# Kernel tuning notes

Hardware: AMD Instinct MI355X
Metric: run time of the kernel (lower is better)

The kernel has to match this reference:

```python
import jax, jax.numpy as jnp
import numpy as np

N = 50000
NEG_SLOPE = 0.2  # PyG GATConv default negative_slope


def _gat_layer(x, src, dst, edge_attr, W, We, a_src, a_dst, a_edge, bias):
    """Single-head PyG GATConv (heads=1, concat=True, add_self_loops=True,
    fill_value='mean' for self-loop edge_attr, dropout inactive / eval mode)."""
    n = x.shape[0]
    # add self loops; self-loop edge_attr = per-feature mean of edge_attr
    loop = jnp.arange(n)
    src2 = jnp.concatenate([src, loop])
    dst2 = jnp.concatenate([dst, loop])
    ea_loop = jnp.broadcast_to(edge_attr.mean(axis=0, keepdims=True), (n, edge_attr.shape[1]))
    ea = jnp.concatenate([edge_attr, ea_loop], axis=0)          # [E', edge_dim]

    h = x @ W                                                    # [N, C_out]
    a_s = h @ a_src                                              # [N]
    a_d = h @ a_dst                                              # [N]
    a_e = (ea @ We) @ a_edge                                     # [E']

    alpha = jax.nn.leaky_relu(a_s[src2] + a_d[dst2] + a_e, NEG_SLOPE)  # [E']
    # segment softmax over incoming edges of each dst node
    amax = jax.ops.segment_max(alpha, dst2, num_segments=n)     # [N]
    ex = jnp.exp(alpha - amax[dst2])                             # [E']
    denom = jax.ops.segment_sum(ex, dst2, num_segments=n)       # [N]
    w = ex / denom[dst2]                                         # [E']

    msg = h[src2] * w[:, None]                                   # [E', C_out]
    out = jax.ops.segment_sum(msg, dst2, num_segments=n) + bias  # [N, C_out]
    return out


def setup_inputs() -> dict:
    key = jax.random.key(0)
    ks = jax.random.split(key, 16)
    E, C_in, C_h, C_out, Ed = 800000, 128, 256, 128, 8
    s = 0.05
    inp = {
        "x": jax.random.normal(ks[0], (N, C_in), dtype=jnp.float32),
        "edge_index": jax.random.randint(ks[1], (2, E), 0, N, dtype=jnp.int32),
        "edge_attr": jax.random.normal(ks[2], (E, Ed), dtype=jnp.float32),
        # layer 1 params
        "W1": jax.random.normal(ks[3], (C_in, C_h), dtype=jnp.float32) * s,
        "We1": jax.random.normal(ks[4], (Ed, C_h), dtype=jnp.float32) * s,
        "as1": jax.random.normal(ks[5], (C_h,), dtype=jnp.float32) * s,
        "ad1": jax.random.normal(ks[6], (C_h,), dtype=jnp.float32) * s,
        "ae1": jax.random.normal(ks[7], (C_h,), dtype=jnp.float32) * s,
        "b1": jnp.zeros((C_h,), dtype=jnp.float32),
        # layer 2 params
        "W2": jax.random.normal(ks[8], (C_h, C_out), dtype=jnp.float32) * s,
        "We2": jax.random.normal(ks[9], (Ed, C_out), dtype=jnp.float32) * s,
        "as2": jax.random.normal(ks[10], (C_out,), dtype=jnp.float32) * s,
        "ad2": jax.random.normal(ks[11], (C_out,), dtype=jnp.float32) * s,
        "ae2": jax.random.normal(ks[12], (C_out,), dtype=jnp.float32) * s,
        "b2": jnp.zeros((C_out,), dtype=jnp.float32),
    }
    return inp


def reference(x, edge_index, edge_attr, W1, We1, as1, ad1, ae1, b1,
              W2, We2, as2, ad2, ae2, b2):
    src, dst = edge_index[0], edge_index[1]
    h = _gat_layer(x, src, dst, edge_attr, W1, We1, as1, ad1, ae1, b1)
    h = jax.nn.relu(h)  # relu between layers, not after last
    out = _gat_layer(h, src, dst, edge_attr, W2, We2, as2, ad2, ae2, b2)
    return out
```

## Files before the change

### kernel.cpp

```cpp
#include <hip/hip_runtime.h>
#include <hip/hip_bf16.h>


#define NEG_SLOPE 0.2f

typedef unsigned short u16;
typedef short short8 __attribute__((ext_vector_type(8)));
typedef float v4f __attribute__((ext_vector_type(4)));
typedef u16 u16x4 __attribute__((ext_vector_type(4)));
typedef u16 u16x8 __attribute__((ext_vector_type(8)));

__device__ __forceinline__ u16 f2bf(float f) {
    unsigned u = __float_as_uint(f);
    return (u16)((u + 0x7fffu + ((u >> 16) & 1u)) >> 16);
}
__device__ __forceinline__ float bf2f(u16 h) {
    return __uint_as_float(((unsigned)h) << 16);
}
__device__ __forceinline__ float bf_lo(int v) { return __uint_as_float(((unsigned)v) << 16); }
__device__ __forceinline__ float bf_hi(int v) { return __uint_as_float(((unsigned)v) & 0xffff0000u); }
__device__ __forceinline__ float lrelu(float x) {
    return x >= 0.f ? x : NEG_SLOPE * x;
}
__device__ __forceinline__ int ld_acq(int* p) {
    return __hip_atomic_load(p, __ATOMIC_ACQUIRE, __HIP_MEMORY_SCOPE_AGENT);
}
__device__ __forceinline__ void st_rel(int* p, int v) {
    __hip_atomic_store(p, v, __ATOMIC_RELEASE, __HIP_MEMORY_SCOPE_AGENT);
}

__global__ __launch_bounds__(256) void prep_kernel(
        const float* __restrict__ W1, u16* __restrict__ w1thi, u16* __restrict__ w1tlo,
        const float* __restrict__ W2, u16* __restrict__ w2thi, u16* __restrict__ w2tlo,
        const float* __restrict__ We1, const float* __restrict__ ae1v,
        const float* __restrict__ We2, const float* __restrict__ ae2v,
        float* __restrict__ we_vec1g, float* __restrict__ we_vec2g) {
    int tid = threadIdx.x;
    if (blockIdx.x < 256) {
        int t = blockIdx.x * 256 + tid;
        if (t < 128 * 256) {
            int k = t >> 8, m = t & 255;
            float v = W1[t];
            u16 h = f2bf(v);
            w1thi[(size_t)m * 128 + k] = h;
            w1tlo[(size_t)m * 128 + k] = f2bf(v - bf2f(h));
        } else {
            t -= 128 * 256;
            int k = t >> 7, m = t & 127;
            float v = W2[t];
            u16 h = f2bf(v);
            w2thi[(size_t)m * 256 + k] = h;
            w2tlo[(size_t)m * 256 + k] = f2bf(v - bf2f(h));
        }
        return;
    }
    __shared__ float wv[16];
    if (tid < 16) wv[tid] = 0.f;
    __syncthreads();
    {
        float a1 = ae1v[tid];
        int lane = tid & 63;
#pragma unroll
        for (int j = 0; j < 8; ++j) {
            float v = We1[j * 256 + tid] * a1;
#pragma unroll
            for (int o = 32; o; o >>= 1) v += __shfl_down(v, o);
            if (lane == 0) atomicAdd(&wv[j], v);
        }
        if (tid < 128) {
            float a2 = ae2v[tid];
#pragma unroll
            for (int j = 0; j < 8; ++j) {
                float v = We2[j * 128 + tid] * a2;
#pragma unroll
                for (int o = 32; o; o >>= 1) v += __shfl_down(v, o);
                if (lane == 0) atomicAdd(&wv[8 + j], v);
            }
        }
    }
    __syncthreads();
    if (tid < 8)  we_vec1g[tid] = wv[tid];
    else if (tid < 16) we_vec2g[tid - 8] = wv[tid];
}

#define BK 32
#define LDA 40
__global__ __launch_bounds__(256) void fat1_kernel(
        const float* __restrict__ ea, const int* __restrict__ dst,
        float* __restrict__ mean_acc, int* __restrict__ deg,
        int* __restrict__ rank, float2* __restrict__ aEe, int E,
        const float* __restrict__ we_vec1g, const float* __restrict__ we_vec2g,
        int Fb, int Gg,
        const float* __restrict__ A32,
        const u16* __restrict__ Bh_g, const u16* __restrict__ Bl_g,
        u16* __restrict__ Cb, int Nrows, int K, int M,
        const float* __restrict__ av, const float* __restrict__ bv,
        float* __restrict__ as_out, float* __restrict__ ad_out, int gx) {
    __shared__ u16 Ah[64 * LDA];
    __shared__ u16 Bh[128 * LDA];
    __shared__ u16 Bl[128 * LDA];
    __shared__ float red[8];
    int tid = threadIdx.x;
    int bid = (int)blockIdx.x;
    int mn = Fb < Gg ? Fb : Gg;
    int hid = -1, gid = -1;
    if (bid < 2 * mn) {
        if ((bid & 1) == 0) hid = bid >> 1; else gid = bid >> 1;
    } else {
        int rem = bid - 2 * mn;
        if (Fb > Gg) hid = mn + rem; else gid = mn + rem;
    }
    if (hid >= 0) {
        float wv[16];
#pragma unroll
        for (int j = 0; j < 8; ++j) { wv[j] = we_vec1g[j]; wv[8 + j] = we_vec2g[j]; }
        if (tid < 8) red[tid] = 0.f;
        __syncthreads();
        float s[8] = {0.f};
        int stride = Fb * 256;
        for (int e = hid * 256 + tid; e < E; e += stride) {
            int d = dst[e];
            const float4 v0 = *(const float4*)&ea[(size_t)e * 8];
            const float4 v1 = *(const float4*)&ea[(size_t)e * 8 + 4];
            s[0] += v0.x; s[1] += v0.y; s[2] += v0.z; s[3] += v0.w;
            s[4] += v1.x; s[5] += v1.y; s[6] += v1.z; s[7] += v1.w;
            float s1 = v0.x * wv[0] + v0.y * wv[1] + v0.z * wv[2] + v0.w * wv[3]
                     + v1.x * wv[4] + v1.y * wv[5] + v1.z * wv[6] + v1.w * wv[7];
            float s2 = v0.x * wv[8] + v0.y * wv[9] + v0.z * wv[10] + v0.w * wv[11]
                     + v1.x * wv[12] + v1.y * wv[13] + v1.z * wv[14] + v1.w * wv[15];
            aEe[e] = make_float2(s1, s2);
            rank[e] = atomicAdd(&deg[d], 1);
        }
        int lane = tid & 63;
#pragma unroll
        for (int j = 0; j < 8; ++j) {
#pragma unroll
            for (int o = 32; o; o >>= 1) s[j] += __shfl_down(s[j], o);
            if (lane == 0) atomicAdd(&red[j], s[j]);
        }
        __syncthreads();
        if (tid < 8) atomicAdd(&mean_acc[tid], red[tid]);
        return;
    }
    int lane = tid & 63;
    int wvx = tid >> 6;
    int l15 = lane & 15, quad = lane >> 4;
    int rb = (gid / gx) * 64;
    int cb = (gid % gx) * 128;

    v4f acc[8];
#pragma unroll
    for (int ni = 0; ni < 8; ++ni) acc[ni] = (v4f){0.f, 0.f, 0.f, 0.f};

    int sr  = tid >> 2;
    int sc  = (tid & 3) * 8;
    int sr2 = tid >> 1;
    int sc2 = (tid & 1) * 16;

    for (int kc = 0; kc < K; kc += BK) {
        int gr = rb + sr;
        u16x8 a0 = {0,0,0,0,0,0,0,0};
        if (gr < Nrows) {
            const float* pa = A32 + (size_t)gr * K + kc + sc;
            float4 f0 = *(const float4*)pa;
            float4 f1 = *(const float4*)(pa + 4);
            a0 = (u16x8){f2bf(f0.x), f2bf(f0.y), f2bf(f0.z), f2bf(f0.w),
                         f2bf(f1.x), f2bf(f1.y), f2bf(f1.z), f2bf(f1.w)};
        }
        size_t bb = (size_t)(cb + sr2) * K + kc + sc2;
        u16x8 b0 = *(const u16x8*)(Bh_g + bb);
        u16x8 b1 = *(const u16x8*)(Bh_g + bb + 8);
        u16x8 b2 = *(const u16x8*)(Bl_g + bb);
        u16x8 b3 = *(const u16x8*)(Bl_g + bb + 8);
        *(u16x8*)&Ah[sr * LDA + sc] = a0;
        *(u16x8*)&Bh[sr2 * LDA + sc2] = b0;
        *(u16x8*)&Bh[sr2 * LDA + sc2 + 8] = b1;
        *(u16x8*)&Bl[sr2 * LDA + sc2] = b2;
        *(u16x8*)&Bl[sr2 * LDA + sc2 + 8] = b3;
        __syncthreads();
        short8 ah = *(const short8*)&Ah[(wvx * 16 + l15) * LDA + quad * 8];
#pragma unroll
        for (int ni = 0; ni < 8; ++ni) {
            int r = (ni * 16 + l15) * LDA + quad * 8;
            short8 bhf = *(const short8*)&Bh[r];
            short8 blf = *(const short8*)&Bl[r];
            acc[ni] = __builtin_amdgcn_mfma_f32_16x16x32_bf16(ah, bhf, acc[ni], 0, 0, 0);
            acc[ni] = __builtin_amdgcn_mfma_f32_16x16x32_bf16(ah, blf, acc[ni], 0, 0, 0);
        }
        __syncthreads();
    }
#pragma unroll
    for (int ni = 0; ni < 8; ++ni)
#pragma unroll
        for (int reg = 0; reg < 4; ++reg) {
            int row = rb + wvx * 16 + quad * 4 + reg;
            if (row < Nrows)
                Cb[(size_t)row * M + cb + ni * 16 + l15] = f2bf(acc[ni][reg]);
        }
    float sd[4] = {}, dd[4] = {};
#pragma unroll
    for (int ni = 0; ni < 8; ++ni) {
        int col = cb + ni * 16 + l15;
        float a = av[col], b = bv[col];
#pragma unroll
        for (int reg = 0; reg < 4; ++reg) {
            sd[reg] += acc[ni][reg] * a;
            dd[reg] += acc[ni][reg] * b;
        }
    }
#pragma unroll
    for (int off = 1; off < 16; off <<= 1)
#pragma unroll
        for (int reg = 0; reg < 4; ++reg) {
            sd[reg] += __shfl_xor(sd[reg], off);
            dd[reg] += __shfl_xor(dd[reg], off);
        }
    if (l15 == 0) {
        int row0 = rb + wvx * 16 + quad * 4;
#pragma unroll
        for (int reg = 0; reg < 4; ++reg)
            if (row0 + reg < Nrows) {
                atomicAdd(as_out + row0 + reg, sd[reg]);
                atomicAdd(ad_out + row0 + reg, dd[reg]);
            }
    }
}

__global__ __launch_bounds__(256) void scan_fused_kernel(
        const int* __restrict__ deg, int* __restrict__ row_start,
        int* __restrict__ partials, int* __restrict__ pprefix,
        int* __restrict__ gcount, int* __restrict__ gflag, int N, int n,
        const float* __restrict__ mean_acc, float Einv,
        const float* __restrict__ we_vec1, const float* __restrict__ we_vec2,
        float* __restrict__ ae_loop) {
    __shared__ int s[256];
    __shared__ int amLast, bprefix;
    int t = threadIdx.x, bid = blockIdx.x;
    int i = bid * 256 + t;
    int v = (i < N) ? deg[i] : 0;
    s[t] = v; __syncthreads();
    for (int off = 1; off < 256; off <<= 1) {
        int u = (t >= off) ? s[t - off] : 0;
        __syncthreads();
        s[t] += u;
        __syncthreads();
    }
    int incl = s[t];
    int total = s[255];
    if (t == 0) {
        partials[bid] = total;
        __threadfence();
        int c = __hip_atomic_fetch_add(gcount, 1, __ATOMIC_ACQ_REL, __HIP_MEMORY_SCOPE_AGENT);
        amLast = (c == (int)gridDim.x - 1);
    }
    __syncthreads();
    if (amLast) {
        int G = gridDim.x;
        int pv = (t < G) ? ld_acq(&partials[t]) : 0;
        __syncthreads();
        s[t] = pv; __syncthreads();
        for (int off = 1; off < 256; off <<= 1) {
            int u = (t >= off) ? s[t - off] : 0;
            __syncthreads();
            s[t] += u;
            __syncthreads();
        }
        if (t < G) pprefix[t] = s[t] - pv;
        if (t == 0) {
            float s1 = 0.f, s2 = 0.f;
#pragma unroll
            for (int j = 0; j < 8; ++j) {
                float m = mean_acc[j] * Einv;
                s1 += m * we_vec1[j];
                s2 += m * we_vec2[j];
            }
            ae_loop[0] = s1; ae_loop[1] = s2;
        }
        __threadfence();
        __syncthreads();
        if (t == 0) st_rel(gflag, 1);
    }
    if (t == 0) {
        while (ld_acq(gflag) == 0) __builtin_amdgcn_s_sleep(2);
        bprefix = ld_acq(&pprefix[bid]);
    }
    __syncthreads();
    int ex = bprefix + incl - v;
    if (i < n) row_start[i] = ex;
}

__global__ __launch_bounds__(256) void fill_kernel(
        const int* __restrict__ src, const int* __restrict__ dst,
        const float2* __restrict__ aEe, const int* __restrict__ row_start,
        const int* __restrict__ rank,
        float4* __restrict__ epack, int E) {
    int e = blockIdx.x * 256 + threadIdx.x;
    if (e >= E) return;
    int d = dst[e];
    int idx = row_start[d] + rank[e];
    float2 a = aEe[e];
    epack[idx] = make_float4(__int_as_float(src[e]), a.x, a.y, 0.f);
}

#define LDA2 40
__global__ __launch_bounds__(256) void gemm_mfma_kernel(
        const u16* __restrict__ A_g,
        const u16* __restrict__ Bh_g, const u16* __restrict__ Bl_g,
        u16* __restrict__ Cb, int Nrows, int K, int M,
        const float* __restrict__ av, const float* __restrict__ bv,
        float* __restrict__ as_out, float* __restrict__ ad_out) {
    __shared__ u16 Ah[128 * LDA2], Bh[128 * LDA2], Bl[128 * LDA2];
    int tid = threadIdx.x;
    int lane = tid & 63;
    int wv = tid >> 6;
    int wm = wv >> 1, wn = wv & 1;
    int l15 = lane & 15, quad = lane >> 4;
    int rb = blockIdx.y * 128;
    int cb = blockIdx.x * 128;

    v4f acc[4][4];
#pragma unroll
    for (int mi = 0; mi < 4; ++mi)
#pragma unroll
        for (int ni = 0; ni < 4; ++ni) acc[mi][ni] = (v4f){0.f, 0.f, 0.f, 0.f};

    int sr = tid >> 1;
    int sc = (tid & 1) * 16;

    for (int kc = 0; kc < K; kc += BK) {
        int gr = rb + sr;
        u16x8 a0 = {0,0,0,0,0,0,0,0}, a1 = {0,0,0,0,0,0,0,0};
        if (gr < Nrows) {
            size_t ba = (size_t)gr * K + kc + sc;
            a0 = *(const u16x8*)(A_g + ba);
            a1 = *(const u16x8*)(A_g + ba + 8);
        }
        size_t bb = (size_t)(cb + sr) * K + kc + sc;
        u16x8 b0 = *(const u16x8*)(Bh_g + bb);
        u16x8 b1 = *(const u16x8*)(Bh_g + bb + 8);
        u16x8 b2 = *(const u16x8*)(Bl_g + bb);
        u16x8 b3 = *(const u16x8*)(Bl_g + bb + 8);
        *(u16x8*)&Ah[sr * LDA2 + sc] = a0;
        *(u16x8*)&Ah[sr * LDA2 + sc + 8] = a1;
        *(u16x8*)&Bh[sr * LDA2 + sc] = b0;
        *(u16x8*)&Bh[sr * LDA2 + sc + 8] = b1;
        *(u16x8*)&Bl[sr * LDA2 + sc] = b2;
        *(u16x8*)&Bl[sr * LDA2 + sc + 8] = b3;
        __syncthreads();
        short8 ah[4], bh[4], bl[4];
#pragma unroll
        for (int mi = 0; mi < 4; ++mi)
            ah[mi] = *(const short8*)&Ah[(wm * 64 + mi * 16 + l15) * LDA2 + quad * 8];
#pragma unroll
        for (int ni = 0; ni < 4; ++ni) {
            int r = (wn * 64 + ni * 16 + l15) * LDA2 + quad * 8;
            bh[ni] = *(const short8*)&Bh[r];
            bl[ni] = *(const short8*)&Bl[r];
        }
#pragma unroll
        for (int mi = 0; mi < 4; ++mi)
#pragma unroll
            for (int ni = 0; ni < 4; ++ni) {
                acc[mi][ni] = __builtin_amdgcn_mfma_f32_16x16x32_bf16(ah[mi], bh[ni], acc[mi][ni], 0, 0, 0);
                acc[mi][ni] = __builtin_amdgcn_mfma_f32_16x16x32_bf16(ah[mi], bl[ni], acc[mi][ni], 0, 0, 0);
            }
        __syncthreads();
    }
#pragma unroll
    for (int mi = 0; mi < 4; ++mi)
#pragma unroll
        for (int ni = 0; ni < 4; ++ni)
#pragma unroll
            for (int reg = 0; reg < 4; ++reg) {
                int row = rb + wm * 64 + mi * 16 + quad * 4 + reg;
                if (row < Nrows)
                    Cb[(size_t)row * M + cb + wn * 64 + ni * 16 + l15] = f2bf(acc[mi][ni][reg]);
            }
    float sd[4][4] = {}, dd[4][4] = {};
#pragma unroll
    for (int ni = 0; ni < 4; ++ni) {
        int col = cb + wn * 64 + ni * 16 + l15;
        float a = av[col], b = bv[col];
#pragma unroll
        for (int mi = 0; mi < 4; ++mi)
#pragma unroll
            for (int reg = 0; reg < 4; ++reg) {
                sd[mi][reg] += acc[mi][ni][reg] * a;
                dd[mi][reg] += acc[mi][ni][reg] * b;
            }
    }
#pragma unroll
    for (int off = 1; off < 16; off <<= 1)
#pragma unroll
        for (int mi = 0; mi < 4; ++mi)
#pragma unroll
            for (int reg = 0; reg < 4; ++reg) {
                sd[mi][reg] += __shfl_xor(sd[mi][reg], off);
                dd[mi][reg] += __shfl_xor(dd[mi][reg], off);
            }
    if (l15 == 0)
#pragma unroll
        for (int mi = 0; mi < 4; ++mi) {
            int row0 = rb + wm * 64 + mi * 16 + quad * 4;
#pragma unroll
            for (int reg = 0; reg < 4; ++reg)
                if (row0 + reg < Nrows) {
                    atomicAdd(as_out + row0 + reg, sd[mi][reg]);
                    atomicAdd(ad_out + row0 + reg, dd[mi][reg]);
                }
        }
}

__global__ __launch_bounds__(256) void agg1_kernel(const int* __restrict__ row_start,
                                                   const float4* __restrict__ epack,
                                                   const float* __restrict__ asv,
                                                   const float* __restrict__ adv,
                                                   const float* __restrict__ ae_loop,
                                                   const u16* __restrict__ Hb,
                                                   u16* __restrict__ ohi,
                                                   const float* __restrict__ bias, int N) {
    __shared__ float2 xch[4][64];
    int lane = threadIdx.x & 63;
    int wvi = threadIdx.x >> 6;
    int node = blockIdx.x * 4 + wvi;
    if (node >= N) return;
    int st = row_start[node], en = row_start[node + 1];
    float ad = adv[node];
    float aloop = lrelu(asv[node] + ad + ae_loop[0]);
    float m = aloop, sum = 1.f;
    float acc0, acc1, acc2, acc3;
    {
        int2 hv = *(const int2*)(Hb + (size_t)node * 256 + lane * 4);
        acc0 = bf_lo(hv.x); acc1 = bf_hi(hv.x);
        acc2 = bf_lo(hv.y); acc3 = bf_hi(hv.y);
    }
    for (int base = st; base < en; base += 64) {
        int i = base + lane;
        float al = -3.0e38f; int sreg = 0;
        if (i < en) {
            float4 ep = epack[i];
            sreg = __float_as_int(ep.x);
            al = lrelu(asv[sreg] + ad + ep.y);
        }
        float cm = al;
#pragma unroll
        for (int o = 1; o < 64; o <<= 1) cm = fmaxf(cm, __shfl_xor(cm, o));
        if (cm > m) {
            float sc = __expf(m - cm);
            acc0 *= sc; acc1 *= sc; acc2 *= sc; acc3 *= sc;
            sum *= sc; m = cm;
        }
        float w = (i < en) ? __expf(al - m) : 0.f;
        float wsum = w;
#pragma unroll
        for (int o = 1; o < 64; o <<= 1) wsum += __shfl_xor(wsum, o);
        sum += wsum;
        xch[wvi][lane] = make_float2(w, __int_as_float(sreg));
        int cnt = min(64, en - base);
        int j = 0;
        for (; j + 8 <= cnt; j += 8) {
            float2 e[8]; int2 h[8];
#pragma unroll
            for (int q = 0; q < 8; ++q) e[q] = xch[wvi][j + q];
#pragma unroll
            for (int q = 0; q < 8; ++q)
                h[q] = *(const int2*)(Hb + (size_t)__float_as_int(e[q].y) * 256 + lane * 4);
#pragma unroll
            for (int q = 0; q < 8; ++q) {
                acc0 += e[q].x * bf_lo(h[q].x); acc1 += e[q].x * bf_hi(h[q].x);
                acc2 += e[q].x * bf_lo(h[q].y); acc3 += e[q].x * bf_hi(h[q].y);
            }
        }
        for (; j + 4 <= cnt; j += 4) {
            float2 e0 = xch[wvi][j], e1 = xch[wvi][j + 1];
            float2 e2 = xch[wvi][j + 2], e3 = xch[wvi][j + 3];
            int2 h0 = *(const int2*)(Hb + (size_t)__float_as_int(e0.y) * 256 + lane * 4);
            int2 h1 = *(const int2*)(Hb + (size_t)__float_as_int(e1.y) * 256 + lane * 4);
            int2 h2 = *(const int2*)(Hb + (size_t)__float_as_int(e2.y) * 256 + lane * 4);
            int2 h3 = *(const int2*)(Hb + (size_t)__float_as_int(e3.y) * 256 + lane * 4);
            acc0 += e0.x * bf_lo(h0.x) + e1.x * bf_lo(h1.x) + e2.x * bf_lo(h2.x) + e3.x * bf_lo(h3.x);
            acc1 += e0.x * bf_hi(h0.x) + e1.x * bf_hi(h1.x) + e2.x * bf_hi(h2.x) + e3.x * bf_hi(h3.x);
            acc2 += e0.x * bf_lo(h0.y) + e1.x * bf_lo(h1.y) + e2.x * bf_lo(h2.y) + e3.x * bf_lo(h3.y);
            acc3 += e0.x * bf_hi(h0.y) + e1.x * bf_hi(h1.y) + e2.x * bf_hi(h2.y) + e3.x * bf_hi(h3.y);
        }
        for (; j < cnt; ++j) {
            float2 e0 = xch[wvi][j];
            int2 h0 = *(const int2*)(Hb + (size_t)__float_as_int(e0.y) * 256 + lane * 4);
            acc0 += e0.x * bf_lo(h0.x); acc1 += e0.x * bf_hi(h0.x);
            acc2 += e0.x * bf_lo(h0.y); acc3 += e0.x * bf_hi(h0.y);
        }
    }
    float inv = 1.f / sum;
    const float4 bvv = *(const float4*)(bias + lane * 4);
    float t0 = acc0 * inv + bvv.x, t1 = acc1 * inv + bvv.y;
    float t2 = acc2 * inv + bvv.z, t3 = acc3 * inv + bvv.w;
    t0 = t0 > 0.f ? t0 : 0.f; t1 = t1 > 0.f ? t1 : 0.f;
    t2 = t2 > 0.f ? t2 : 0.f; t3 = t3 > 0.f ? t3 : 0.f;
    u16x4 h;
    h.x = f2bf(t0); h.y = f2bf(t1); h.z = f2bf(t2); h.w = f2bf(t3);
    *(u16x4*)(ohi + (size_t)node * 256 + lane * 4) = h;
}

__global__ __launch_bounds__(256) void agg2_kernel(const int* __restrict__ row_start,
                                                   const float4* __restrict__ epack,
                                                   const float* __restrict__ asv,
                                                   const float* __restrict__ adv,
                                                   const float* __restrict__ ae_loop,
                                                   const u16* __restrict__ Hb,
                                                   float* __restrict__ out,
                                                   const float* __restrict__ bias, int N) {
    __shared__ float2 xch[4][64];
    int lane = threadIdx.x & 63;
    int wvi = threadIdx.x >> 6;
    int node = blockIdx.x * 4 + wvi;
    if (node >= N) return;
    int st = row_start[node], en = row_start[node + 1];
    float ad = adv[node];
    float aloop = lrelu(asv[node] + ad + ae_loop[1]);
    float m = aloop, sum = 1.f;
    float acc0, acc1;
    {
        int hv = *(const int*)(Hb + (size_t)node * 128 + lane * 2);
        acc0 = bf_lo(hv); acc1 = bf_hi(hv);
    }
    for (int base = st; base < en; base += 64) {
        int i = base + lane;
        float al = -3.0e38f; int sreg = 0;
        if (i < en) {
            float4 ep = epack[i];
            sreg = __float_as_int(ep.x);
            al = lrelu(asv[sreg] + ad + ep.z);
        }
        float cm = al;
#pragma unroll
        for (int o = 1; o < 64; o <<= 1) cm = fmaxf(cm, __shfl_xor(cm, o));
        if (cm > m) {
            float sc = __expf(m - cm);
            acc0 *= sc; acc1 *= sc;
            sum *= sc; m = cm;
        }
        float w = (i < en) ? __expf(al - m) : 0.f;
        float wsum = w;
#pragma unroll
        for (int o = 1; o < 64; o <<= 1) wsum += __shfl_xor(wsum, o);
        sum += wsum;
        xch[wvi][lane] = make_float2(w, __int_as_float(sreg));
        int cnt = min(64, en - base);
        int j = 0;
        for (; j + 8 <= cnt; j += 8) {
            float2 e[8]; int h[8];
#pragma unroll
            for (int q = 0; q < 8; ++q) e[q] = xch[wvi][j + q];
#pragma unroll
            for (int q = 0; q < 8; ++q)
                h[q] = *(const int*)(Hb + (size_t)__float_as_int(e[q].y) * 128 + lane * 2);
#pragma unroll
            for (int q = 0; q < 8; ++q) {
                acc0 += e[q].x * bf_lo(h[q]); acc1 += e[q].x * bf_hi(h[q]);
            }
        }
        for (; j + 4 <= cnt; j += 4) {
            float2 e0 = xch[wvi][j], e1 = xch[wvi][j + 1];
            float2 e2 = xch[wvi][j + 2], e3 = xch[wvi][j + 3];
            int h0 = *(const int*)(Hb + (size_t)__float_as_int(e0.y) * 128 + lane * 2);
            int h1 = *(const int*)(Hb + (size_t)__float_as_int(e1.y) * 128 + lane * 2);
            int h2 = *(const int*)(Hb + (size_t)__float_as_int(e2.y) * 128 + lane * 2);
            int h3 = *(const int*)(Hb + (size_t)__float_as_int(e3.y) * 128 + lane * 2);
            acc0 += e0.x * bf_lo(h0) + e1.x * bf_lo(h1) + e2.x * bf_lo(h2) + e3.x * bf_lo(h3);
            acc1 += e0.x * bf_hi(h0) + e1.x * bf_hi(h1) + e2.x * bf_hi(h2) + e3.x * bf_hi(h3);
        }
        for (; j < cnt; ++j) {
            float2 e0 = xch[wvi][j];
            int h0 = *(const int*)(Hb + (size_t)__float_as_int(e0.y) * 128 + lane * 2);
            acc0 += e0.x * bf_lo(h0); acc1 += e0.x * bf_hi(h0);
        }
    }
    float inv = 1.f / sum;
    size_t o = (size_t)node * 128 + lane * 2;
    out[o]     = acc0 * inv + bias[lane * 2];
    out[o + 1] = acc1 * inv + bias[lane * 2 + 1];
}

extern "C" void kernel_launch(void* const* d_in, const int* in_sizes, int n_in,
                              void* d_out, int out_size, void* d_ws, size_t ws_size,
                              hipStream_t stream) {
    const int Cin = 128, Ch = 256, Co = 128;
    const int N = in_sizes[0] / Cin;
    const int E = in_sizes[1] / 2;

    const float* x   = (const float*)d_in[0];
    const int*   src = (const int*)d_in[1];
    const int*   dst = src + E;
    const float* ea  = (const float*)d_in[2];
    const float* W1  = (const float*)d_in[3];
    const float* We1 = (const float*)d_in[4];
    const float* as1 = (const float*)d_in[5];
    const float* ad1 = (const float*)d_in[6];
    const float* ae1 = (const float*)d_in[7];
    const float* b1  = (const float*)d_in[8];
    const float* W2  = (const float*)d_in[9];
    const float* We2 = (const float*)d_in[10];
    const float* as2 = (const float*)d_in[11];
    const float* ad2 = (const float*)d_in[12];
    const float* ae2 = (const float*)d_in[13];
    const float* b2  = (const float*)d_in[14];
    float* out = (float*)d_out;

    float* ws = (float*)d_ws;
    size_t off = 0;
    u16* h1b = (u16*)(ws + off); off += (size_t)N * Ch / 2;
    u16* g1b = (u16*)(ws + off); off += (size_t)N * Ch / 2;
    float4* epack = (float4*)(ws + off); off += (size_t)E * 4;
    float2* aEe   = (float2*)(ws + off); off += (size_t)E * 2;
    int* rank     = (int*)(ws + off); off += (size_t)E;
    int* row_start = (int*)(ws + off); off += (size_t)N + 1;
    int* partials  = (int*)(ws + off); off += 256;
    int* pprefix   = (int*)(ws + off); off += 256;
    u16* w1thi = (u16*)(ws + off); off += (size_t)Cin * Ch / 2;
    u16* w1tlo = (u16*)(ws + off); off += (size_t)Cin * Ch / 2;
    u16* w2thi = (u16*)(ws + off); off += (size_t)Ch * Co / 2;
    u16* w2tlo = (u16*)(ws + off); off += (size_t)Ch * Co / 2;
    int*   deg  = (int*)(ws + off); off += (size_t)N + 1;
    float* asv1 = ws + off; off += (size_t)N;
    float* adv1 = ws + off; off += (size_t)N;
    float* asv2 = ws + off; off += (size_t)N;
    float* adv2 = ws + off; off += (size_t)N;
    float* misc = ws + off; off += 32;
    float* mean_acc = misc;
    float* we_vec1  = misc + 8;
    float* we_vec2  = misc + 16;
    float* ae_loop  = misc + 24;
    int* gcount = (int*)(ws + off); off += 1;
    int* gflag  = (int*)(ws + off); off += 1;

    const int n1 = N + 1;
    const int nscan = (n1 + 255) / 256;

    hipMemsetAsync(deg, 0, ((size_t)5 * N + 35) * sizeof(float), stream);

    prep_kernel<<<257, 256, 0, stream>>>(
        W1, w1thi, w1tlo, W2, w2thi, w2tlo,
        We1, ae1, We2, ae2, we_vec1, we_vec2);

    {
        int Fb = 1024;
        int gx = Ch / 128;
        int Gg = gx * ((N + 63) / 64);
        fat1_kernel<<<Fb + Gg, 256, 0, stream>>>(
            ea, dst, mean_acc, deg, rank, aEe, E, we_vec1, we_vec2, Fb, Gg,
            x, w1thi, w1tlo, h1b, N, Cin, Ch, as1, ad1, asv1, adv1, gx);
    }

    scan_fused_kernel<<<nscan, 256, 0, stream>>>(
        deg, row_start, partials, pprefix, gcount, gflag, N, n1,
        mean_acc, 1.0f / (float)E, we_vec1, we_vec2, ae_loop);

    fill_kernel<<<(E + 255) / 256, 256, 0, stream>>>(src, dst, aEe, row_start,
                                                     rank, epack, E);

    agg1_kernel<<<(N + 3) / 4, 256, 0, stream>>>(row_start, epack, asv1, adv1, ae_loop,
                                                 h1b, g1b, b1, N);

    u16* h2b = h1b;
    {
        dim3 grid(Co / 128, (N + 127) / 128);
        gemm_mfma_kernel<<<grid, 256, 0, stream>>>(g1b, w2thi, w2tlo, h2b, N, Ch, Co,
                                                   as2, ad2, asv2, adv2);
    }
    agg2_kernel<<<(N + 3) / 4, 256, 0, stream>>>(row_start, epack, asv2, adv2, ae_loop,
                                                 h2b, out, b2, N);
}
```

Measured before the change: 349.8 us.

## Drop online softmax max, precompute layer-1 edge weights in fill, split waves into halves

The running-max online softmax in both aggregation kernels is replaced by a plain exp-sum, which removes the per-chunk max shuffle reduction and the rescaling of accumulators. The layer-1 edge weights exp(lrelu(...)) are now computed once in fill_kernel and stored in epack, so agg1 reads them directly. Each wave is split into two 32-lane halves that gather alternate neighbours with wider vector loads (int4 or int2), and the halves are combined with one cross-half shuffle at the end. Skipping max subtraction risks overflow in exp if attention logits are large, though the small parameter scale probably keeps them bounded.

```diff
diff --git a/kernel.cpp b/kernel.cpp
--- a/kernel.cpp
+++ b/kernel.cpp
@@ -7,7 +7,6 @@
 typedef unsigned short u16;
 typedef short short8 __attribute__((ext_vector_type(8)));
 typedef float v4f __attribute__((ext_vector_type(4)));
-typedef u16 u16x4 __attribute__((ext_vector_type(4)));
 typedef u16 u16x8 __attribute__((ext_vector_type(8)));
 
 __device__ __forceinline__ u16 f2bf(float f) {
@@ -293,13 +292,16 @@
         const int* __restrict__ src, const int* __restrict__ dst,
         const float2* __restrict__ aEe, const int* __restrict__ row_start,
         const int* __restrict__ rank,
+        const float* __restrict__ asv1, const float* __restrict__ adv1,
         float4* __restrict__ epack, int E) {
     int e = blockIdx.x * 256 + threadIdx.x;
     if (e >= E) return;
     int d = dst[e];
+    int s = src[e];
     int idx = row_start[d] + rank[e];
     float2 a = aEe[e];
-    epack[idx] = make_float4(__int_as_float(src[e]), a.x, a.y, 0.f);
+    float w = __expf(lrelu(asv1[s] + adv1[d] + a.x));
+    epack[idx] = make_float4(__int_as_float(s), w, a.y, 0.f);
 }
 
 #define LDA2 40
@@ -425,32 +427,27 @@
     int node = blockIdx.x * 4 + wvi;
     if (node >= N) return;
     int st = row_start[node], en = row_start[node + 1];
-    float ad = adv[node];
-    float aloop = lrelu(asv[node] + ad + ae_loop[0]);
-    float m = aloop, sum = 1.f;
-    float acc0, acc1, acc2, acc3;
+    float wloop = __expf(lrelu(asv[node] + adv[node] + ae_loop[0]));
+    float sum = wloop;
+    int half = lane >> 5;
+    int hl   = lane & 31;
+    float acc[8];
     {
-        int2 hv = *(const int2*)(Hb + (size_t)node * 256 + lane * 4);
-        acc0 = bf_lo(hv.x); acc1 = bf_hi(hv.x);
-        acc2 = bf_lo(hv.y); acc3 = bf_hi(hv.y);
+        int4 hv = *(const int4*)(Hb + (size_t)node * 256 + hl * 8);
+        float w0 = half ? 0.f : wloop;
+        acc[0] = w0 * bf_lo(hv.x); acc[1] = w0 * bf_hi(hv.x);
+        acc[2] = w0 * bf_lo(hv.y); acc[3] = w0 * bf_hi(hv.y);
+        acc[4] = w0 * bf_lo(hv.z); acc[5] = w0 * bf_hi(hv.z);
+        acc[6] = w0 * bf_lo(hv.w); acc[7] = w0 * bf_hi(hv.w);
     }
     for (int base = st; base < en; base += 64) {
         int i = base + lane;
-        float al = -3.0e38f; int sreg = 0;
+        float w = 0.f; int sreg = 0;
         if (i < en) {
             float4 ep = epack[i];
             sreg = __float_as_int(ep.x);
-            al = lrelu(asv[sreg] + ad + ep.y);
-        }
-        float cm = al;
-#pragma unroll
-        for (int o = 1; o < 64; o <<= 1) cm = fmaxf(cm, __shfl_xor(cm, o));
-        if (cm > m) {
-            float sc = __expf(m - cm);
-            acc0 *= sc; acc1 *= sc; acc2 *= sc; acc3 *= sc;
-            sum *= sc; m = cm;
-        }
-        float w = (i < en) ? __expf(al - m) : 0.f;
+            w = ep.y;
+        }
         float wsum = w;
 #pragma unroll
         for (int o = 1; o < 64; o <<= 1) wsum += __shfl_xor(wsum, o);
@@ -459,46 +456,59 @@
         int cnt = min(64, en - base);
         int j = 0;
         for (; j + 8 <= cnt; j += 8) {
-            float2 e[8]; int2 h[8];
-#pragma unroll
-            for (int q = 0; q < 8; ++q) e[q] = xch[wvi][j + q];
-#pragma unroll
-            for (int q = 0; q < 8; ++q)
-                h[q] = *(const int2*)(Hb + (size_t)__float_as_int(e[q].y) * 256 + lane * 4);
-#pragma unroll
-            for (int q = 0; q < 8; ++q) {
-                acc0 += e[q].x * bf_lo(h[q].x); acc1 += e[q].x * bf_hi(h[q].x);
-                acc2 += e[q].x * bf_lo(h[q].y); acc3 += e[q].x * bf_hi(h[q].y);
-            }
-        }
-        for (; j + 4 <= cnt; j += 4) {
-            float2 e0 = xch[wvi][j], e1 = xch[wvi][j + 1];
-            float2 e2 = xch[wvi][j + 2], e3 = xch[wvi][j + 3];
-            int2 h0 = *(const int2*)(Hb + (size_t)__float_as_int(e0.y) * 256 + lane * 4);
-            int2 h1 = *(const int2*)(Hb + (size_t)__float_as_int(e1.y) * 256 + lane * 4);
-            int2 h2 = *(const int2*)(Hb + (size_t)__float_as_int(e2.y) * 256 + lane * 4);
-            int2 h3 = *(const int2*)(Hb + (size_t)__float_as_int(e3.y) * 256 + lane * 4);
-            acc0 += e0.x * bf_lo(h0.x) + e1.x * bf_lo(h1.x) + e2.x * bf_lo(h2.x) + e3.x * bf_lo(h3.x);
-            acc1 += e0.x * bf_hi(h0.x) + e1.x * bf_hi(h1.x) + e2.x * bf_hi(h2.x) + e3.x * bf_hi(h3.x);
-            acc2 += e0.x * bf_lo(h0.y) + e1.x * bf_lo(h1.y) + e2.x * bf_lo(h2.y) + e3.x * bf_lo(h3.y);
-            acc3 += e0.x * bf_hi(h0.y) + e1.x * bf_hi(h1.y) + e2.x * bf_hi(h2.y) + e3.x * bf_hi(h3.y);
-        }
-        for (; j < cnt; ++j) {
+            float2 e[4]; int4 h[4];
+#pragma unroll
+            for (int q = 0; q < 4; ++q) e[q] = xch[wvi][j + 2 * q + half];
+#pragma unroll
+            for (int q = 0; q < 4; ++q)
+                h[q] = *(const int4*)(Hb + (size_t)__float_as_int(e[q].y) * 256 + hl * 8);
+#pragma unroll
+            for (int q = 0; q < 4; ++q) {
+                float w0 = e[q].x;
+                acc[0] += w0 * bf_lo(h[q].x); acc[1] += w0 * bf_hi(h[q].x);
+                acc[2] += w0 * bf_lo(h[q].y); acc[3] += w0 * bf_hi(h[q].y);
+                acc[4] += w0 * bf_lo(h[q].z); acc[5] += w0 * bf_hi(h[q].z);
+                acc[6] += w0 * bf_lo(h[q].w); acc[7] += w0 * bf_hi(h[q].w);
+            }
+        }
+        for (; j + 2 <= cnt; j += 2) {
+            float2 e0 = xch[wvi][j + half];
+            int4 h0 = *(const int4*)(Hb + (size_t)__float_as_int(e0.y) * 256 + hl * 8);
+            float w0 = e0.x;
+            acc[0] += w0 * bf_lo(h0.x); acc[1] += w0 * bf_hi(h0.x);
+            acc[2] += w0 * bf_lo(h0.y); acc[3] += w0 * bf_hi(h0.y);
+            acc[4] += w0 * bf_lo(h0.z); acc[5] += w0 * bf_hi(h0.z);
+            acc[6] += w0 * bf_lo(h0.w); acc[7] += w0 * bf_hi(h0.w);
+        }
+        if (j < cnt && half == 0) {
             float2 e0 = xch[wvi][j];
-            int2 h0 = *(const int2*)(Hb + (size_t)__float_as_int(e0.y) * 256 + lane * 4);
-            acc0 += e0.x * bf_lo(h0.x); acc1 += e0.x * bf_hi(h0.x);
-            acc2 += e0.x * bf_lo(h0.y); acc3 += e0.x * bf_hi(h0.y);
-        }
-    }
-    float inv = 1.f / sum;
-    const float4 bvv = *(const float4*)(bias + lane * 4);
-    float t0 = acc0 * inv + bvv.x, t1 = acc1 * inv + bvv.y;
-    float t2 = acc2 * inv + bvv.z, t3 = acc3 * inv + bvv.w;
-    t0 = t0 > 0.f ? t0 : 0.f; t1 = t1 > 0.f ? t1 : 0.f;
-    t2 = t2 > 0.f ? t2 : 0.f; t3 = t3 > 0.f ? t3 : 0.f;
-    u16x4 h;
-    h.x = f2bf(t0); h.y = f2bf(t1); h.z = f2bf(t2); h.w = f2bf(t3);
-    *(u16x4*)(ohi + (size_t)node * 256 + lane * 4) = h;
+            int4 h0 = *(const int4*)(Hb + (size_t)__float_as_int(e0.y) * 256 + hl * 8);
+            float w0 = e0.x;
+            acc[0] += w0 * bf_lo(h0.x); acc[1] += w0 * bf_hi(h0.x);
+            acc[2] += w0 * bf_lo(h0.y); acc[3] += w0 * bf_hi(h0.y);
+            acc[4] += w0 * bf_lo(h0.z); acc[5] += w0 * bf_hi(h0.z);
+            acc[6] += w0 * bf_lo(h0.w); acc[7] += w0 * bf_hi(h0.w);
+        }
+    }
+#pragma unroll
+    for (int c = 0; c < 8; ++c) acc[c] += __shfl_xor(acc[c], 32);
+    if (half == 0) {
+        float inv = 1.f / sum;
+        const float4 b0 = *(const float4*)(bias + hl * 8);
+        const float4 b1 = *(const float4*)(bias + hl * 8 + 4);
+        float t0 = acc[0] * inv + b0.x, t1 = acc[1] * inv + b0.y;
+        float t2 = acc[2] * inv + b0.z, t3 = acc[3] * inv + b0.w;
+        float t4 = acc[4] * inv + b1.x, t5 = acc[5] * inv + b1.y;
+        float t6 = acc[6] * inv + b1.z, t7 = acc[7] * inv + b1.w;
+        t0 = t0 > 0.f ? t0 : 0.f; t1 = t1 > 0.f ? t1 : 0.f;
+        t2 = t2 > 0.f ? t2 : 0.f; t3 = t3 > 0.f ? t3 : 0.f;
+        t4 = t4 > 0.f ? t4 : 0.f; t5 = t5 > 0.f ? t5 : 0.f;
+        t6 = t6 > 0.f ? t6 : 0.f; t7 = t7 > 0.f ? t7 : 0.f;
+        u16x8 h;
+        h[0] = f2bf(t0); h[1] = f2bf(t1); h[2] = f2bf(t2); h[3] = f2bf(t3);
+        h[4] = f2bf(t4); h[5] = f2bf(t5); h[6] = f2bf(t6); h[7] = f2bf(t7);
+        *(u16x8*)(ohi + (size_t)node * 256 + hl * 8) = h;
+    }
 }
 
 __global__ __launch_bounds__(256) void agg2_kernel(const int* __restrict__ row_start,
@@ -516,30 +526,25 @@
     if (node >= N) return;
     int st = row_start[node], en = row_start[node + 1];
     float ad = adv[node];
-    float aloop = lrelu(asv[node] + ad + ae_loop[1]);
-    float m = aloop, sum = 1.f;
-    float acc0, acc1;
+    float wloop = __expf(lrelu(asv[node] + ad + ae_loop[1]));
+    float sum = wloop;
+    int half = lane >> 5;
+    int hl   = lane & 31;
+    float acc[4];
     {
-        int hv = *(const int*)(Hb + (size_t)node * 128 + lane * 2);
-        acc0 = bf_lo(hv); acc1 = bf_hi(hv);
+        int2 hv = *(const int2*)(Hb + (size_t)node * 128 + hl * 4);
+        float w0 = half ? 0.f : wloop;
+        acc[0] = w0 * bf_lo(hv.x); acc[1] = w0 * bf_hi(hv.x);
+        acc[2] = w0 * bf_lo(hv.y); acc[3] = w0 * bf_hi(hv.y);
     }
     for (int base = st; base < en; base += 64) {
         int i = base + lane;
-        float al = -3.0e38f; int sreg = 0;
+        float w = 0.f; int sreg = 0;
         if (i < en) {
             float4 ep = epack[i];
             sreg = __float_as_int(ep.x);
-            al = lrelu(asv[sreg] + ad + ep.z);
-        }
-        float cm = al;
-#pragma unroll
-        for (int o = 1; o < 64; o <<= 1) cm = fmaxf(cm, __shfl_xor(cm, o));
-        if (cm > m) {
-            float sc = __expf(m - cm);
-            acc0 *= sc; acc1 *= sc;
-            sum *= sc; m = cm;
-        }
-        float w = (i < en) ? __expf(al - m) : 0.f;
+            w = __expf(lrelu(asv[sreg] + ad + ep.z));
+        }
         float wsum = w;
 #pragma unroll
         for (int o = 1; o < 64; o <<= 1) wsum += __shfl_xor(wsum, o);
@@ -548,37 +553,46 @@
         int cnt = min(64, en - base);
         int j = 0;
         for (; j + 8 <= cnt; j += 8) {
-            float2 e[8]; int h[8];
-#pragma unroll
-            for (int q = 0; q < 8; ++q) e[q] = xch[wvi][j + q];
-#pragma unroll
-            for (int q = 0; q < 8; ++q)
-                h[q] = *(const int*)(Hb + (size_t)__float_as_int(e[q].y) * 128 + lane * 2);
-#pragma unroll
-            for (int q = 0; q < 8; ++q) {
-                acc0 += e[q].x * bf_lo(h[q]); acc1 += e[q].x * bf_hi(h[q]);
-            }
-        }
-        for (; j + 4 <= cnt; j += 4) {
-            float2 e0 = xch[wvi][j], e1 = xch[wvi][j + 1];
-            float2 e2 = xch[wvi][j + 2], e3 = xch[wvi][j + 3];
-            int h0 = *(const int*)(Hb + (size_t)__float_as_int(e0.y) * 128 + lane * 2);
-            int h1 = *(const int*)(Hb + (size_t)__float_as_int(e1.y) * 128 + lane * 2);
-            int h2 = *(const int*)(Hb + (size_t)__float_as_int(e2.y) * 128 + lane * 2);
-            int h3 = *(const int*)(Hb + (size_t)__float_as_int(e3.y) * 128 + lane * 2);
-            acc0 += e0.x * bf_lo(h0) + e1.x * bf_lo(h1) + e2.x * bf_lo(h2) + e3.x * bf_lo(h3);
-            acc1 += e0.x * bf_hi(h0) + e1.x * bf_hi(h1) + e2.x * bf_hi(h2) + e3.x * bf_hi(h3);
-        }
-        for (; j < cnt; ++j) {
+            float2 e[4]; int2 h[4];
+#pragma unroll
+            for (int q = 0; q < 4; ++q) e[q] = xch[wvi][j + 2 * q + half];
+#pragma unroll
+            for (int q = 0; q < 4; ++q)
+                h[q] = *(const int2*)(Hb + (size_t)__float_as_int(e[q].y) * 128 + hl * 4);
+#pragma unroll
+            for (int q = 0; q < 4; ++q) {
+                float w0 = e[q].x;
+                acc[0] += w0 * bf_lo(h[q].x); acc[1] += w0 * bf_hi(h[q].x);
+                acc[2] += w0 * bf_lo(h[q].y); acc[3] += w0 * bf_hi(h[q].y);
+            }
+        }
+        for (; j + 2 <= cnt; j += 2) {
+            float2 e0 = xch[wvi][j + half];
+            int2 h0 = *(const int2*)(Hb + (size_t)__float_as_int(e0.y) * 128 + hl * 4);
+            float w0 = e0.x;
+            acc[0] += w0 * bf_lo(h0.x); acc[1] += w0 * bf_hi(h0.x);
+            acc[2] += w0 * bf_lo(h0.y); acc[3] += w0 * bf_hi(h0.y);
+        }
+        if (j < cnt && half == 0) {
             float2 e0 = xch[wvi][j];
-            int h0 = *(const int*)(Hb + (size_t)__float_as_int(e0.y) * 128 + lane * 2);
-            acc0 += e0.x * bf_lo(h0); acc1 += e0.x * bf_hi(h0);
-        }
-    }
-    float inv = 1.f / sum;
-    size_t o = (size_t)node * 128 + lane * 2;
-    out[o]     = acc0 * inv + bias[lane * 2];
-    out[o + 1] = acc1 * inv + bias[lane * 2 + 1];
+            int2 h0 = *(const int2*)(Hb + (size_t)__float_as_int(e0.y) * 128 + hl * 4);
+            float w0 = e0.x;
+            acc[0] += w0 * bf_lo(h0.x); acc[1] += w0 * bf_hi(h0.x);
+            acc[2] += w0 * bf_lo(h0.y); acc[3] += w0 * bf_hi(h0.y);
+        }
+    }
+#pragma unroll
+    for (int c = 0; c < 4; ++c) acc[c] += __shfl_xor(acc[c], 32);
+    if (half == 0) {
+        float inv = 1.f / sum;
+        const float4 bv = *(const float4*)(bias + hl * 4);
+        float4 o;
+        o.x = acc[0] * inv + bv.x;
+        o.y = acc[1] * inv + bv.y;
+        o.z = acc[2] * inv + bv.z;
+        o.w = acc[3] * inv + bv.w;
+        *(float4*)(out + (size_t)node * 128 + hl * 4) = o;
+    }
 }
 
 extern "C" void kernel_launch(void* const* d_in, const int* in_sizes, int n_in,
@@ -656,7 +670,7 @@
         mean_acc, 1.0f / (float)E, we_vec1, we_vec2, ae_loop);
 
     fill_kernel<<<(E + 255) / 256, 256, 0, stream>>>(src, dst, aEe, row_start,
-                                                     rank, epack, E);
+                                                     rank, asv1, adv1, epack, E);
 
     agg1_kernel<<<(N + 3) / 4, 256, 0, stream>>>(row_start, epack, asv1, adv1, ae_loop,
                                                  h1b, g1b, b1, N);
```

Result: no change. 343.6 us, median of 2 (-1.8%).
